# Kernel tuning notes

Measured on AMD Instinct MI355X. Metric: run time of the kernel, lower is better.

Reference implementation:

```python
import jax, jax.numpy as jnp
import numpy as np

NUM_STEPS = 8  # fixed-step RK4 stand-in for adaptive DormandPrince(atol=1e-5)
B, D, C, H = 8192, 508, 1, 256
DIN = D + C + 1  # state + conditional + time


def _mlp(h, w0, b0, w1, b1, w2, b2):
    h = jnp.tanh(h @ w0 + b0)
    h = jnp.tanh(h @ w1 + b1)
    return h @ w2 + b2


def setup_inputs() -> dict:
    key = jax.random.key(0)
    ks = jax.random.split(key, 6)
    sc = lambda k, shape, fan: jax.random.normal(k, shape, jnp.float32) / np.sqrt(fan)
    return {
        "x": jax.random.normal(ks[0], (B, D), jnp.float32),
        "cond": jax.random.uniform(ks[1], (B, C), jnp.float32),
        "eps": jax.random.normal(ks[2], (B, D), jnp.float32),  # Hutchinson probe
        "w0": sc(ks[3], (DIN, H), DIN),
        "b0": jnp.zeros((H,), jnp.float32),
        "w1": sc(ks[4], (H, H), H),
        "b1": jnp.zeros((H,), jnp.float32),
        "w2": sc(ks[5], (H, D), H),
        "b2": jnp.zeros((D,), jnp.float32),
    }


def reference(x, cond, eps, w0, b0, w1, b1, w2, b2):
    """FFJORD bijector forward: integrate dx/dt = f(t, x, cond) from t=0 to 1
    with augmented Hutchinson trace estimate d(logdet)/dt = eps^T (df/dx) eps.
    Returns (y, log_det_jacobian_estimate)."""
    dt = jnp.float32(1.0 / NUM_STEPS)

    def dyn(t, y):
        def f(y_):
            tcol = jnp.full((y_.shape[0], 1), t, y_.dtype)
            return _mlp(jnp.concatenate([y_, cond, tcol], axis=-1),
                        w0, b0, w1, b1, w2, b2)
        fy, vjp_fn = jax.vjp(f, y)
        (etJ,) = vjp_fn(eps)           # eps^T J
        tr = jnp.sum(etJ * eps, -1)    # eps^T J eps  -> [B]
        return fy, tr

    def step(carry, i):
        y, ld = carry
        t = i * dt
        k1, l1 = dyn(t, y)
        k2, l2 = dyn(t + 0.5 * dt, y + 0.5 * dt * k1)
        k3, l3 = dyn(t + 0.5 * dt, y + 0.5 * dt * k2)
        k4, l4 = dyn(t + dt, y + dt * k3)
        y = y + (dt / 6.0) * (k1 + 2.0 * k2 + 2.0 * k3 + k4)
        ld = ld + (dt / 6.0) * (l1 + 2.0 * l2 + 2.0 * l3 + l4)
        return (y, ld), None

    init = (x, jnp.zeros((x.shape[0],), x.dtype))
    (y, ld), _ = jax.lax.scan(step, init, jnp.arange(NUM_STEPS, dtype=x.dtype))
    return y, ld
```

## Files before the change

### kernel.cpp

```cpp
#include <hip/hip_runtime.h>
#include <math.h>

namespace {

constexpr int Bn = 8192;
constexpr int Dn = 508;
constexpr int Hn = 256;
constexpr int NSTEPS = 8;
constexpr int Kp = 512;
constexpr float DT = 1.f / NSTEPS;
constexpr float DT6 = DT / 6.f;

typedef __attribute__((ext_vector_type(8))) short short8v;
typedef __attribute__((ext_vector_type(4))) float f32x4;

__device__ __forceinline__ short f2b(float f) {
  union { float f; unsigned u; } v; v.f = f;
  unsigned r = v.u + 0x7fffu + ((v.u >> 16) & 1u);
  return (short)(r >> 16);
}
__device__ __forceinline__ float b2f(short s) {
  union { unsigned u; float f; } v;
  v.u = ((unsigned)(unsigned short)s) << 16;
  return v.f;
}
__device__ __forceinline__ unsigned pk2(short lo, short hi) {
  return ((unsigned)(unsigned short)lo) | (((unsigned)(unsigned short)hi) << 16);
}
__device__ __forceinline__ float upk_lo(unsigned p) {
  union { unsigned u; float f; } v; v.u = p << 16; return v.f;
}
__device__ __forceinline__ float upk_hi(unsigned p) {
  union { unsigned u; float f; } v; v.u = p & 0xffff0000u; return v.f;
}
__device__ __forceinline__ float ftanh(float x) {
  const float e = __expf(2.f * x);
  return 1.f - __fdividef(2.f, 1.f + e);
}

template <int KT>
__device__ __forceinline__ void gemm_bb(const short* __restrict__ A, int lda,
                                        const short* __restrict__ Bt, int ldb,
                                        int row0, int col0, int lane,
                                        f32x4 acc[2][2]) {
  const int r = lane & 15, g = lane >> 4;
  const short* a0p = A + (size_t)(row0 + r) * lda + g * 8;
  const short* a1p = A + (size_t)(row0 + 16 + r) * lda + g * 8;
  const short* b0p = Bt + (size_t)(col0 + r) * ldb + g * 8;
  const short* b1p = Bt + (size_t)(col0 + 16 + r) * ldb + g * 8;
#pragma unroll
  for (int kt = 0; kt < KT; ++kt) {
    const short8v a0 = *(const short8v*)(a0p + kt * 32);
    const short8v a1 = *(const short8v*)(a1p + kt * 32);
    const short8v b0 = *(const short8v*)(b0p + kt * 32);
    const short8v b1 = *(const short8v*)(b1p + kt * 32);
    acc[0][0] = __builtin_amdgcn_mfma_f32_16x16x32_bf16(a0, b0, acc[0][0], 0, 0, 0);
    acc[0][1] = __builtin_amdgcn_mfma_f32_16x16x32_bf16(a0, b1, acc[0][1], 0, 0, 0);
    acc[1][0] = __builtin_amdgcn_mfma_f32_16x16x32_bf16(a1, b0, acc[1][0], 0, 0, 0);
    acc[1][1] = __builtin_amdgcn_mfma_f32_16x16x32_bf16(a1, b1, acc[1][1], 0, 0, 0);
  }
}

#define GEMM_PROLOGUE()                                     \
  const int tid = threadIdx.x, wid = tid >> 6, lane = tid & 63; \
  const int row0 = blockIdx.y * 64 + (wid >> 1) * 32;       \
  const int col0 = blockIdx.x * 64 + (wid & 1) * 32;        \
  const int rq = (lane >> 4) * 4, cc = lane & 15;           \
  const f32x4 z4 = {0.f, 0.f, 0.f, 0.f};                    \
  f32x4 acc[2][2] = {{z4, z4}, {z4, z4}};


__global__ __launch_bounds__(256) void k_cast_bf(const float* __restrict__ src, int R,
                                                 int C, short* __restrict__ dst, int ldd) {
  const int total = R * ldd;
  for (int idx = blockIdx.x * 256 + threadIdx.x; idx < total; idx += gridDim.x * 256) {
    const int r = idx / ldd, c = idx - r * ldd;
    dst[idx] = (c < C) ? f2b(src[(size_t)r * C + c]) : (short)0;
  }
}

__global__ __launch_bounds__(256) void k_transpose_bf(const float* __restrict__ src, int K,
                                                      int N, short* __restrict__ dst,
                                                      int Nd, int ldd) {
  const int total = Nd * ldd;
  for (int idx = blockIdx.x * 256 + threadIdx.x; idx < total; idx += gridDim.x * 256) {
    const int n = idx / ldd, k = idx - n * ldd;
    dst[idx] = (k < K && n < N) ? f2b(src[(size_t)k * N + n]) : (short)0;
  }
}

__global__ __launch_bounds__(256) void k_c0(const float* __restrict__ w0,
                                            const float* __restrict__ b2,
                                            float* __restrict__ c0) {
  const int n = threadIdx.x;
  float s = 0.f;
#pragma unroll 8
  for (int d = 0; d < Dn; ++d) s += b2[d] * w0[(size_t)d * Hn + n];
  c0[n] = s;
}

__global__ __launch_bounds__(256) void k_w20t(const short* __restrict__ w0T,
                                              const short* __restrict__ w2b,
                                              short* __restrict__ w20T) {
  GEMM_PROLOGUE();
  gemm_bb<16>(w0T, Kp, w2b, Kp, row0, col0, lane, acc);
#pragma unroll
  for (int i = 0; i < 2; ++i)
#pragma unroll
    for (int j = 0; j < 2; ++j)
#pragma unroll
      for (int q = 0; q < 4; ++q)
        w20T[(size_t)(row0 + i * 16 + rq + q) * Hn + col0 + j * 16 + cc] =
            f2b(acc[i][j][q]);
}

__global__ __launch_bounds__(256) void k_ginitx(const float* __restrict__ Af,
                                                const short* __restrict__ Bt,
                                                const float* __restrict__ cond,
                                                const float* __restrict__ w0c,
                                                float* __restrict__ zout) {
  GEMM_PROLOGUE();
  const int g = lane >> 4;
  const float* a0r = Af + (size_t)(row0 + cc) * Dn;
  const float* a1r = Af + (size_t)(row0 + 16 + cc) * Dn;
  const short* b0p = Bt + (size_t)(col0 + cc) * Kp + g * 8;
  const short* b1p = Bt + (size_t)(col0 + 16 + cc) * Kp + g * 8;
#pragma unroll
  for (int kt = 0; kt < 16; ++kt) {
    const int k = kt * 32 + g * 8;
    short8v a0v, a1v;
#pragma unroll
    for (int h = 0; h < 2; ++h) {
      const int k4 = k + h * 4;
      float4 fa = make_float4(0.f, 0.f, 0.f, 0.f);
      float4 fb = make_float4(0.f, 0.f, 0.f, 0.f);
      if (k4 < Dn) {
        fa = *(const float4*)(a0r + k4);
        fb = *(const float4*)(a1r + k4);
      }
      a0v[h * 4 + 0] = f2b(fa.x); a0v[h * 4 + 1] = f2b(fa.y);
      a0v[h * 4 + 2] = f2b(fa.z); a0v[h * 4 + 3] = f2b(fa.w);
      a1v[h * 4 + 0] = f2b(fb.x); a1v[h * 4 + 1] = f2b(fb.y);
      a1v[h * 4 + 2] = f2b(fb.z); a1v[h * 4 + 3] = f2b(fb.w);
    }
    const short8v b0v = *(const short8v*)(b0p + kt * 32);
    const short8v b1v = *(const short8v*)(b1p + kt * 32);
    acc[0][0] = __builtin_amdgcn_mfma_f32_16x16x32_bf16(a0v, b0v, acc[0][0], 0, 0, 0);
    acc[0][1] = __builtin_amdgcn_mfma_f32_16x16x32_bf16(a0v, b1v, acc[0][1], 0, 0, 0);
    acc[1][0] = __builtin_amdgcn_mfma_f32_16x16x32_bf16(a1v, b0v, acc[1][0], 0, 0, 0);
    acc[1][1] = __builtin_amdgcn_mfma_f32_16x16x32_bf16(a1v, b1v, acc[1][1], 0, 0, 0);
  }
#pragma unroll
  for (int i = 0; i < 2; ++i)
#pragma unroll
    for (int j = 0; j < 2; ++j)
#pragma unroll
      for (int q = 0; q < 4; ++q) {
        const int row = row0 + i * 16 + rq + q;
        const int col = col0 + j * 16 + cc;
        zout[(size_t)row * Hn + col] = acc[i][j][q] + cond[row] * w0c[col];
      }
}

__global__ __launch_bounds__(256) void k_giniteps(const float* __restrict__ Af,
                                                  const short* __restrict__ BtU,
                                                  const short* __restrict__ BtG,
                                                  short* __restrict__ uout,
                                                  short* __restrict__ gout) {
  GEMM_PROLOGUE();
  f32x4 acc2[2][2] = {{z4, z4}, {z4, z4}};
  const int g = lane >> 4;
  const float* a0r = Af + (size_t)(row0 + cc) * Dn;
  const float* a1r = Af + (size_t)(row0 + 16 + cc) * Dn;
  const short* u0p = BtU + (size_t)(col0 + cc) * Kp + g * 8;
  const short* u1p = BtU + (size_t)(col0 + 16 + cc) * Kp + g * 8;
  const short* g0p = BtG + (size_t)(col0 + cc) * Kp + g * 8;
  const short* g1p = BtG + (size_t)(col0 + 16 + cc) * Kp + g * 8;
#pragma unroll
  for (int kt = 0; kt < 16; ++kt) {
    const int k = kt * 32 + g * 8;
    short8v a0v, a1v;
#pragma unroll
    for (int h = 0; h < 2; ++h) {
      const int k4 = k + h * 4;
      float4 fa = make_float4(0.f, 0.f, 0.f, 0.f);
      float4 fb = make_float4(0.f, 0.f, 0.f, 0.f);
      if (k4 < Dn) {
        fa = *(const float4*)(a0r + k4);
        fb = *(const float4*)(a1r + k4);
      }
      a0v[h * 4 + 0] = f2b(fa.x); a0v[h * 4 + 1] = f2b(fa.y);
      a0v[h * 4 + 2] = f2b(fa.z); a0v[h * 4 + 3] = f2b(fa.w);
      a1v[h * 4 + 0] = f2b(fb.x); a1v[h * 4 + 1] = f2b(fb.y);
      a1v[h * 4 + 2] = f2b(fb.z); a1v[h * 4 + 3] = f2b(fb.w);
    }
    const short8v bu0 = *(const short8v*)(u0p + kt * 32);
    const short8v bu1 = *(const short8v*)(u1p + kt * 32);
    const short8v bg0 = *(const short8v*)(g0p + kt * 32);
    const short8v bg1 = *(const short8v*)(g1p + kt * 32);
    acc[0][0] = __builtin_amdgcn_mfma_f32_16x16x32_bf16(a0v, bu0, acc[0][0], 0, 0, 0);
    acc[0][1] = __builtin_amdgcn_mfma_f32_16x16x32_bf16(a0v, bu1, acc[0][1], 0, 0, 0);
    acc[1][0] = __builtin_amdgcn_mfma_f32_16x16x32_bf16(a1v, bu0, acc[1][0], 0, 0, 0);
    acc[1][1] = __builtin_amdgcn_mfma_f32_16x16x32_bf16(a1v, bu1, acc[1][1], 0, 0, 0);
    acc2[0][0] = __builtin_amdgcn_mfma_f32_16x16x32_bf16(a0v, bg0, acc2[0][0], 0, 0, 0);
    acc2[0][1] = __builtin_amdgcn_mfma_f32_16x16x32_bf16(a0v, bg1, acc2[0][1], 0, 0, 0);
    acc2[1][0] = __builtin_amdgcn_mfma_f32_16x16x32_bf16(a1v, bg0, acc2[1][0], 0, 0, 0);
    acc2[1][1] = __builtin_amdgcn_mfma_f32_16x16x32_bf16(a1v, bg1, acc2[1][1], 0, 0, 0);
  }
#pragma unroll
  for (int i = 0; i < 2; ++i)
#pragma unroll
    for (int j = 0; j < 2; ++j)
#pragma unroll
      for (int q = 0; q < 4; ++q) {
        const int row = row0 + i * 16 + rq + q;
        const int col = col0 + j * 16 + cc;
        uout[(size_t)row * Hn + col] = f2b(acc[i][j][q]);
        gout[(size_t)row * Hn + col] = f2b(acc2[i][j][q]);
      }
}

__global__ __launch_bounds__(256) void k_fragpack(const short* __restrict__ src,
                                                  short* __restrict__ dst, int total) {
  for (int idx = blockIdx.x * 256 + threadIdx.x; idx < total; idx += gridDim.x * 256) {
    const int j = idx & 7;
    const int l = (idx >> 3) & 63;
    const int ks = (idx >> 9) & 7;
    const int c16 = idx >> 12;
    dst[idx] = src[(size_t)(c16 * 16 + (l & 15)) * 256 + ks * 32 + (l >> 4) * 8 + j];
  }
}


__device__ __forceinline__ int swz(int row, int col) {
  return (row * 256 + col) ^ ((row & 7) << 3);
}

constexpr int HP = 257;

__global__ __launch_bounds__(512) void k_mega(
    const float* __restrict__ zg, const short* __restrict__ u_g,
    const short* __restrict__ g2_g, const short* __restrict__ w1P,
    const short* __restrict__ w20P, const short* __restrict__ w2P,
    const float* __restrict__ b0, const float* __restrict__ w0t,
    const float* __restrict__ b1, const float* __restrict__ c0,
    const float* __restrict__ b2, const float* __restrict__ x,
    float* __restrict__ yout, float* __restrict__ ldout) {
  __shared__ short As[32 * 256];
  __shared__ short h1s[16 * 256];
  __shared__ float kzpL[16 * HP];
  __shared__ float kzaL[16 * HP];
  __shared__ float red[16][8];

  const int tid = threadIdx.x;
  const int w = tid >> 6, lane = tid & 63;
  const int cc = lane & 15, g = lane >> 4, rq = g * 4;
  const int r0 = blockIdx.x * 16;
  const int cb = w * 32;

  float b0c[2], w0tc[2], b1c[2], c0c[2];
#pragma unroll
  for (int nt = 0; nt < 2; ++nt) {
    const int col = cb + nt * 16 + cc;
    b0c[nt] = b0[col];
    w0tc[nt] = w0t[col];
    b1c[nt] = b1[col];
    c0c[nt] = c0[col];
  }

  const short* w1base = w1P + (size_t)(2 * w) * 4096 + lane * 8;
  const short* w20base = w20P + (size_t)(2 * w) * 4096 + lane * 8;

  const size_t gbase = (size_t)(r0 + rq) * Hn + cb + cc;

  float z_[2][4], hs[2][4], tr_[4];
  unsigned u_pk[2][2], g2_pk[2][2];
#pragma unroll
  for (int nt = 0; nt < 2; ++nt) {
    const size_t i0 = gbase + nt * 16;
#pragma unroll
    for (int q = 0; q < 4; ++q) {
      z_[nt][q] = zg[i0 + (size_t)q * Hn];
      hs[nt][q] = 0.f;
    }
    u_pk[nt][0] = pk2(u_g[i0], u_g[i0 + Hn]);
    u_pk[nt][1] = pk2(u_g[i0 + 2 * Hn], u_g[i0 + 3 * Hn]);
    g2_pk[nt][0] = pk2(g2_g[i0], g2_g[i0 + Hn]);
    g2_pk[nt][1] = pk2(g2_g[i0 + 2 * Hn], g2_g[i0 + 3 * Hn]);
  }
#pragma unroll
  for (int q = 0; q < 4; ++q) tr_[q] = 0.f;

  for (int i = tid; i < 16 * HP; i += 512) kzpL[i] = 0.f;
  __syncthreads();

  const f32x4 zero4 = {0.f, 0.f, 0.f, 0.f};

#pragma unroll 1
  for (int e = 0; e < 4 * NSTEPS; ++e) {
    const int j = e & 3, s = e >> 2;
    const float oj = (j == 0) ? 0.f : ((j == 3) ? 1.f : 0.5f);
    const float aj = (j == 0) ? 0.f : ((j == 3) ? DT : 0.5f * DT);
    const float mj = (j == 1 || j == 2) ? 2.f : 1.f;
    const float tval = ((float)s + oj) * DT;

#pragma unroll
    for (int nt = 0; nt < 2; ++nt)
#pragma unroll
      for (int q = 0; q < 4; ++q) {
        const int row = rq + q;
        const int colh = cb + nt * 16 + cc;
        const float pre =
            z_[nt][q] + aj * kzpL[row * HP + colh] + b0c[nt] + tval * w0tc[nt];
        const float h = ftanh(pre);
        const float uq = (q & 1) ? upk_hi(u_pk[nt][q >> 1]) : upk_lo(u_pk[nt][q >> 1]);
        As[swz(row, colh)] = f2b(h);
        As[swz(16 + row, colh)] = f2b((1.f - h * h) * uq);
      }
    __syncthreads();

    {
      f32x4 acc[2][2] = {{zero4, zero4}, {zero4, zero4}};
#pragma unroll
      for (int ks = 0; ks < 8; ++ks) {
        const short8v b0v = *(const short8v*)(w1base + ks * 512);
        const short8v b1v = *(const short8v*)(w1base + 4096 + ks * 512);
        const short8v a0 = *(const short8v*)(As + swz(cc, g * 8 + ks * 32));
        const short8v a1 = *(const short8v*)(As + swz(16 + cc, g * 8 + ks * 32));
        acc[0][0] = __builtin_amdgcn_mfma_f32_16x16x32_bf16(a0, b0v, acc[0][0], 0, 0, 0);
        acc[0][1] = __builtin_amdgcn_mfma_f32_16x16x32_bf16(a0, b1v, acc[0][1], 0, 0, 0);
        acc[1][0] = __builtin_amdgcn_mfma_f32_16x16x32_bf16(a1, b0v, acc[1][0], 0, 0, 0);
        acc[1][1] = __builtin_amdgcn_mfma_f32_16x16x32_bf16(a1, b1v, acc[1][1], 0, 0, 0);
      }
#pragma unroll
      for (int nt = 0; nt < 2; ++nt)
#pragma unroll
        for (int q = 0; q < 4; ++q) {
          const float v = ftanh(acc[0][nt][q] + b1c[nt]);
          const float g2q =
              (q & 1) ? upk_hi(g2_pk[nt][q >> 1]) : upk_lo(g2_pk[nt][q >> 1]);
          tr_[q] += (DT6 * mj) * g2q * (1.f - v * v) * acc[1][nt][q];
          h1s[swz(rq + q, cb + nt * 16 + cc)] = f2b(v);
          hs[nt][q] += mj * v;
        }
    }
    __syncthreads();

    {
      f32x4 acc2[2] = {zero4, zero4};
#pragma unroll
      for (int ks = 0; ks < 8; ++ks) {
        const short8v b0v = *(const short8v*)(w20base + ks * 512);
        const short8v b1v = *(const short8v*)(w20base + 4096 + ks * 512);
        const short8v a = *(const short8v*)(h1s + swz(cc, g * 8 + ks * 32));
        acc2[0] = __builtin_amdgcn_mfma_f32_16x16x32_bf16(a, b0v, acc2[0], 0, 0, 0);
        acc2[1] = __builtin_amdgcn_mfma_f32_16x16x32_bf16(a, b1v, acc2[1], 0, 0, 0);
      }
#pragma unroll
      for (int nt = 0; nt < 2; ++nt)
#pragma unroll
        for (int q = 0; q < 4; ++q) {
          const float kzv = acc2[nt][q] + c0c[nt];
          const int idx = (rq + q) * HP + cb + nt * 16 + cc;
          if (j == 0) {
            kzaL[idx] = kzv;
            kzpL[idx] = kzv;
          } else if (j < 3) {
            kzaL[idx] += mj * kzv;
            kzpL[idx] = kzv;
          } else {
            z_[nt][q] += DT6 * (kzaL[idx] + kzv);
          }
        }
    }
  }

#pragma unroll
  for (int nt = 0; nt < 2; ++nt)
#pragma unroll
    for (int q = 0; q < 4; ++q)
      As[swz(rq + q, cb + nt * 16 + cc)] = f2b(hs[nt][q]);
  __syncthreads();
  {
    const short* w2base = w2P + (size_t)(4 * w) * 4096 + lane * 8;
    f32x4 facc[4] = {zero4, zero4, zero4, zero4};
#pragma unroll
    for (int ks = 0; ks < 8; ++ks) {
      const short8v a = *(const short8v*)(As + swz(cc, g * 8 + ks * 32));
#pragma unroll
      for (int nt = 0; nt < 4; ++nt) {
        const short8v bv = *(const short8v*)(w2base + nt * 4096 + ks * 512);
        facc[nt] = __builtin_amdgcn_mfma_f32_16x16x32_bf16(a, bv, facc[nt], 0, 0, 0);
      }
    }
#pragma unroll
    for (int nt = 0; nt < 4; ++nt) {
      const int colo = w * 64 + nt * 16 + cc;
      if (colo < Dn) {
        const float b2c = b2[colo];
#pragma unroll
        for (int q = 0; q < 4; ++q) {
          const size_t ix = (size_t)(r0 + rq + q) * Dn + colo;
          yout[ix] = x[ix] + DT6 * facc[nt][q] + b2c;
        }
      }
    }
  }

#pragma unroll
  for (int q = 0; q < 4; ++q) {
    float v = tr_[q];
    v += __shfl_xor(v, 1);
    v += __shfl_xor(v, 2);
    v += __shfl_xor(v, 4);
    v += __shfl_xor(v, 8);
    if (cc == 0) red[rq + q][w] = v;
  }
  __syncthreads();
  if (tid < 16) {
    float t = 0.f;
#pragma unroll
    for (int ww = 0; ww < 8; ++ww) t += red[tid][ww];
    ldout[r0 + tid] = t;
  }
}

}

extern "C" void kernel_launch(void* const* d_in, const int* in_sizes, int n_in,
                              void* d_out, int out_size, void* d_ws, size_t ws_size,
                              hipStream_t stream) {
  const float* x = (const float*)d_in[0];
  const float* cond = (const float*)d_in[1];
  const float* eps = (const float*)d_in[2];
  const float* w0 = (const float*)d_in[3];
  const float* b0 = (const float*)d_in[4];
  const float* w1 = (const float*)d_in[5];
  const float* b1 = (const float*)d_in[6];
  const float* w2 = (const float*)d_in[7];
  const float* b2 = (const float*)d_in[8];
  const float* w0c = w0 + (size_t)508 * Hn;
  const float* w0t = w0 + (size_t)509 * Hn;

  const size_t BD = (size_t)Bn * Dn, BH = (size_t)Bn * Hn;
  char* p = (char*)d_ws;
  auto alloc_f = [&](size_t n) { float* r = (float*)p; p += n * 4; return r; };
  auto alloc_s = [&](size_t n) { short* r = (short*)p; p += ((n * 2 + 15) & ~15ull); return r; };

  float* zg = alloc_f(BH);
  float* c0 = alloc_f(256);
  short* u_g = alloc_s(BH);
  short* g2_g = alloc_s(BH);
  short* w0T = alloc_s(256 * 512);
  short* w1T = alloc_s(256 * 256);
  short* w2b = alloc_s(256 * 512);
  short* w2T = alloc_s(512 * 256);
  short* w20T = alloc_s(256 * 256);
  short* w1P = alloc_s(256 * 256);
  short* w20P = alloc_s(256 * 256);
  short* w2P = alloc_s(512 * 256);

  float* yout = (float*)d_out;
  float* ldout = (float*)d_out + BD;

  const dim3 blk(256);
  const dim3 gH(Hn / 64, Bn / 64);
  const dim3 gW(4, 4);

  k_cast_bf<<<512, blk, 0, stream>>>(w2, Hn, Dn, w2b, Kp);
  k_transpose_bf<<<256, blk, 0, stream>>>(w1, Hn, Hn, w1T, Hn, Hn);
  k_transpose_bf<<<512, blk, 0, stream>>>(w0, Dn, Hn, w0T, Hn, Kp);
  k_transpose_bf<<<512, blk, 0, stream>>>(w2, Hn, Dn, w2T, Kp, Hn);
  k_c0<<<1, blk, 0, stream>>>(w0, b2, c0);
  k_w20t<<<gW, blk, 0, stream>>>(w0T, w2b, w20T);
  k_ginitx<<<gH, blk, 0, stream>>>(x, w0T, cond, w0c, zg);
  k_giniteps<<<gH, blk, 0, stream>>>(eps, w0T, w2b, u_g, g2_g);
  k_fragpack<<<256, blk, 0, stream>>>(w1T, w1P, 256 * 256);
  k_fragpack<<<256, blk, 0, stream>>>(w20T, w20P, 256 * 256);
  k_fragpack<<<512, blk, 0, stream>>>(w2T, w2P, 512 * 256);

  k_mega<<<dim3(Bn / 16), dim3(512), 0, stream>>>(zg, u_g, g2_g, w1P, w20P,
                                                  w2P, b0, w0t, b1, c0, b2, x,
                                                  yout, ldout);
}
```

Measured before the change: 315.0 us.

## Halve mega-kernel block to 4 waves, each covering 64 hidden columns

The fused RK4 kernel now runs with 256 threads per block instead of 512. Each wave owns 64 hidden columns rather than 32, so it loads more weight fragments and issues more MFMAs per shared A fragment. The running sum of hidden activations moves from registers into a new shared-memory array to limit register pressure, and the final output GEMM is split into two batches per wave. The aim is more A-operand reuse and fewer waves to synchronise at each barrier. In exchange it costs extra LDS (a third 16x258 float array plus a padding change), extra LDS read-modify-write traffic per stage, and possibly lower occupancy.

```diff
diff --git a/kernel.cpp b/kernel.cpp
--- a/kernel.cpp
+++ b/kernel.cpp
@@ -236,9 +236,9 @@
   return (row * 256 + col) ^ ((row & 7) << 3);
 }
 
-constexpr int HP = 257;
-
-__global__ __launch_bounds__(512) void k_mega(
+constexpr int HP = 258;
+
+__global__ __launch_bounds__(256) void k_mega(
     const float* __restrict__ zg, const short* __restrict__ u_g,
     const short* __restrict__ g2_g, const short* __restrict__ w1P,
     const short* __restrict__ w20P, const short* __restrict__ w2P,
@@ -248,19 +248,20 @@
     float* __restrict__ yout, float* __restrict__ ldout) {
   __shared__ short As[32 * 256];
   __shared__ short h1s[16 * 256];
+  __shared__ float hsum[16 * HP];
   __shared__ float kzpL[16 * HP];
   __shared__ float kzaL[16 * HP];
-  __shared__ float red[16][8];
+  __shared__ float red[16][4];
 
   const int tid = threadIdx.x;
   const int w = tid >> 6, lane = tid & 63;
   const int cc = lane & 15, g = lane >> 4, rq = g * 4;
   const int r0 = blockIdx.x * 16;
-  const int cb = w * 32;
-
-  float b0c[2], w0tc[2], b1c[2], c0c[2];
-#pragma unroll
-  for (int nt = 0; nt < 2; ++nt) {
+  const int cb = w * 64;
+
+  float b0c[4], w0tc[4], b1c[4], c0c[4];
+#pragma unroll
+  for (int nt = 0; nt < 4; ++nt) {
     const int col = cb + nt * 16 + cc;
     b0c[nt] = b0[col];
     w0tc[nt] = w0t[col];
@@ -268,21 +269,18 @@
     c0c[nt] = c0[col];
   }
 
-  const short* w1base = w1P + (size_t)(2 * w) * 4096 + lane * 8;
-  const short* w20base = w20P + (size_t)(2 * w) * 4096 + lane * 8;
+  const short* w1base = w1P + (size_t)(4 * w) * 4096 + lane * 8;
+  const short* w20base = w20P + (size_t)(4 * w) * 4096 + lane * 8;
 
   const size_t gbase = (size_t)(r0 + rq) * Hn + cb + cc;
 
-  float z_[2][4], hs[2][4], tr_[4];
-  unsigned u_pk[2][2], g2_pk[2][2];
-#pragma unroll
-  for (int nt = 0; nt < 2; ++nt) {
+  float z_[4][4], tr_[4];
+  unsigned u_pk[4][2], g2_pk[4][2];
+#pragma unroll
+  for (int nt = 0; nt < 4; ++nt) {
     const size_t i0 = gbase + nt * 16;
 #pragma unroll
-    for (int q = 0; q < 4; ++q) {
-      z_[nt][q] = zg[i0 + (size_t)q * Hn];
-      hs[nt][q] = 0.f;
-    }
+    for (int q = 0; q < 4; ++q) z_[nt][q] = zg[i0 + (size_t)q * Hn];
     u_pk[nt][0] = pk2(u_g[i0], u_g[i0 + Hn]);
     u_pk[nt][1] = pk2(u_g[i0 + 2 * Hn], u_g[i0 + 3 * Hn]);
     g2_pk[nt][0] = pk2(g2_g[i0], g2_g[i0 + Hn]);
@@ -291,7 +289,10 @@
 #pragma unroll
   for (int q = 0; q < 4; ++q) tr_[q] = 0.f;
 
-  for (int i = tid; i < 16 * HP; i += 512) kzpL[i] = 0.f;
+  for (int i = tid; i < 16 * HP; i += 256) {
+    hsum[i] = 0.f;
+    kzpL[i] = 0.f;
+  }
   __syncthreads();
 
   const f32x4 zero4 = {0.f, 0.f, 0.f, 0.f};
@@ -305,7 +306,7 @@
     const float tval = ((float)s + oj) * DT;
 
 #pragma unroll
-    for (int nt = 0; nt < 2; ++nt)
+    for (int nt = 0; nt < 4; ++nt)
 #pragma unroll
       for (int q = 0; q < 4; ++q) {
         const int row = rq + q;
@@ -320,44 +321,47 @@
     __syncthreads();
 
     {
-      f32x4 acc[2][2] = {{zero4, zero4}, {zero4, zero4}};
+      f32x4 acc[2][4] = {{zero4, zero4, zero4, zero4}, {zero4, zero4, zero4, zero4}};
 #pragma unroll
       for (int ks = 0; ks < 8; ++ks) {
-        const short8v b0v = *(const short8v*)(w1base + ks * 512);
-        const short8v b1v = *(const short8v*)(w1base + 4096 + ks * 512);
         const short8v a0 = *(const short8v*)(As + swz(cc, g * 8 + ks * 32));
         const short8v a1 = *(const short8v*)(As + swz(16 + cc, g * 8 + ks * 32));
-        acc[0][0] = __builtin_amdgcn_mfma_f32_16x16x32_bf16(a0, b0v, acc[0][0], 0, 0, 0);
-        acc[0][1] = __builtin_amdgcn_mfma_f32_16x16x32_bf16(a0, b1v, acc[0][1], 0, 0, 0);
-        acc[1][0] = __builtin_amdgcn_mfma_f32_16x16x32_bf16(a1, b0v, acc[1][0], 0, 0, 0);
-        acc[1][1] = __builtin_amdgcn_mfma_f32_16x16x32_bf16(a1, b1v, acc[1][1], 0, 0, 0);
-      }
-#pragma unroll
-      for (int nt = 0; nt < 2; ++nt)
+#pragma unroll
+        for (int nt = 0; nt < 4; ++nt) {
+          const short8v bv = *(const short8v*)(w1base + nt * 4096 + ks * 512);
+          acc[0][nt] = __builtin_amdgcn_mfma_f32_16x16x32_bf16(a0, bv, acc[0][nt], 0, 0, 0);
+          acc[1][nt] = __builtin_amdgcn_mfma_f32_16x16x32_bf16(a1, bv, acc[1][nt], 0, 0, 0);
+        }
+      }
+#pragma unroll
+      for (int nt = 0; nt < 4; ++nt)
 #pragma unroll
         for (int q = 0; q < 4; ++q) {
           const float v = ftanh(acc[0][nt][q] + b1c[nt]);
           const float g2q =
               (q & 1) ? upk_hi(g2_pk[nt][q >> 1]) : upk_lo(g2_pk[nt][q >> 1]);
           tr_[q] += (DT6 * mj) * g2q * (1.f - v * v) * acc[1][nt][q];
-          h1s[swz(rq + q, cb + nt * 16 + cc)] = f2b(v);
-          hs[nt][q] += mj * v;
+          const int row = rq + q;
+          const int colh = cb + nt * 16 + cc;
+          h1s[swz(row, colh)] = f2b(v);
+          hsum[row * HP + colh] += mj * v;
         }
     }
     __syncthreads();
 
     {
-      f32x4 acc2[2] = {zero4, zero4};
+      f32x4 acc2[4] = {zero4, zero4, zero4, zero4};
 #pragma unroll
       for (int ks = 0; ks < 8; ++ks) {
-        const short8v b0v = *(const short8v*)(w20base + ks * 512);
-        const short8v b1v = *(const short8v*)(w20base + 4096 + ks * 512);
         const short8v a = *(const short8v*)(h1s + swz(cc, g * 8 + ks * 32));
-        acc2[0] = __builtin_amdgcn_mfma_f32_16x16x32_bf16(a, b0v, acc2[0], 0, 0, 0);
-        acc2[1] = __builtin_amdgcn_mfma_f32_16x16x32_bf16(a, b1v, acc2[1], 0, 0, 0);
-      }
-#pragma unroll
-      for (int nt = 0; nt < 2; ++nt)
+#pragma unroll
+        for (int nt = 0; nt < 4; ++nt) {
+          const short8v bv = *(const short8v*)(w20base + nt * 4096 + ks * 512);
+          acc2[nt] = __builtin_amdgcn_mfma_f32_16x16x32_bf16(a, bv, acc2[nt], 0, 0, 0);
+        }
+      }
+#pragma unroll
+      for (int nt = 0; nt < 4; ++nt)
 #pragma unroll
         for (int q = 0; q < 4; ++q) {
           const float kzv = acc2[nt][q] + c0c[nt];
@@ -376,14 +380,19 @@
   }
 
 #pragma unroll
-  for (int nt = 0; nt < 2; ++nt)
-#pragma unroll
-    for (int q = 0; q < 4; ++q)
-      As[swz(rq + q, cb + nt * 16 + cc)] = f2b(hs[nt][q]);
+  for (int nt = 0; nt < 4; ++nt)
+#pragma unroll
+    for (int q = 0; q < 4; ++q) {
+      const int row = rq + q;
+      const int colh = cb + nt * 16 + cc;
+      As[swz(row, colh)] = f2b(hsum[row * HP + colh]);
+    }
   __syncthreads();
-  {
-    const short* w2base = w2P + (size_t)(4 * w) * 4096 + lane * 8;
+#pragma unroll 1
+  for (int batch = 0; batch < 2; ++batch) {
     f32x4 facc[4] = {zero4, zero4, zero4, zero4};
+    const short* w2base =
+        w2P + (size_t)(8 * w + batch * 4) * 4096 + lane * 8;
 #pragma unroll
     for (int ks = 0; ks < 8; ++ks) {
       const short8v a = *(const short8v*)(As + swz(cc, g * 8 + ks * 32));
@@ -395,7 +404,7 @@
     }
 #pragma unroll
     for (int nt = 0; nt < 4; ++nt) {
-      const int colo = w * 64 + nt * 16 + cc;
+      const int colo = w * 128 + batch * 64 + nt * 16 + cc;
       if (colo < Dn) {
         const float b2c = b2[colo];
 #pragma unroll
@@ -420,7 +429,7 @@
   if (tid < 16) {
     float t = 0.f;
 #pragma unroll
-    for (int ww = 0; ww < 8; ++ww) t += red[tid][ww];
+    for (int ww = 0; ww < 4; ++ww) t += red[tid][ww];
     ldout[r0 + tid] = t;
   }
 }
@@ -479,7 +488,7 @@
   k_fragpack<<<256, blk, 0, stream>>>(w20T, w20P, 256 * 256);
   k_fragpack<<<512, blk, 0, stream>>>(w2T, w2P, 512 * 256);
 
-  k_mega<<<dim3(Bn / 16), dim3(512), 0, stream>>>(zg, u_g, g2_g, w1P, w20P,
+  k_mega<<<dim3(Bn / 16), dim3(256), 0, stream>>>(zg, u_g, g2_g, w1P, w20P,
                                                   w2P, b0, w0t, b1, c0, b2, x,
                                                   yout, ldout);
 }
```

Measured after the change: 450.3 us. 1.43x slower.
